# Performance work log

Measured on AMD Instinct MI355X. Metric: run time of the kernel, lower is better.

The kernel has to match this reference:

```python
import jax, jax.numpy as jnp
import numpy as np

HEAD_DIM = 64
R = 4            # region_token_num
THETA = 10000.0


def _rope_cos_sin(pos, D, theta):
    # pos: [B, L] int -> cos/sin [B, 1, L, D] (half-split / GPT-NeoX layout)
    inv_freq = theta ** (-(jnp.arange(0, D, 2, dtype=jnp.float32) / D))  # [D/2]
    ang = pos.astype(jnp.float32)[..., None] * inv_freq                  # [B, L, D/2]
    cos = jnp.concatenate([jnp.cos(ang), jnp.cos(ang)], axis=-1)[:, None]
    sin = jnp.concatenate([jnp.sin(ang), jnp.sin(ang)], axis=-1)[:, None]
    return cos, sin


def _apply_rope(x, cos, sin):
    # x: [B, H, L, D]
    D = x.shape[-1]
    x1, x2 = x[..., : D // 2], x[..., D // 2 :]
    rot = jnp.concatenate([-x2, x1], axis=-1)
    return x * cos + rot * sin


def _local_positions(regions):
    # index within contiguous region run: [B, T]
    B, T = regions.shape
    idx = jnp.arange(T, dtype=jnp.int32)
    is_new = jnp.concatenate(
        [jnp.ones((B, 1), bool), regions[:, 1:] != regions[:, :-1]], axis=1
    )
    start = jax.lax.cummax(jnp.where(is_new, idx[None, :], 0), axis=1)
    return idx[None, :] - start


def reference(query_q, x_k, x_v, regions, t_mask, n_mask, max_n):
    B, H, P, D = query_q.shape
    T = regions.shape[1]

    # ---- local RoPE positions: pool tokens all 0 (use_pool_offset=False),
    # x tokens: local index within region + R, zeroed on pads
    pool_pos = jnp.zeros((B, P), dtype=jnp.int32)
    x_pos = (_local_positions(regions) + R) * (regions > 0).astype(jnp.int32)

    cq, sq = _rope_cos_sin(pool_pos, D, THETA)
    ck, sk = _rope_cos_sin(x_pos, D, THETA)
    q = _apply_rope(query_q, cq, sq)
    k = _apply_rope(x_k, ck, sk)

    # ---- block-diagonal (same-region) cross-attention mask [B, 1, P, T]
    pool_region = jnp.repeat(jnp.arange(1, max_n + 1, dtype=regions.dtype), R)  # [P]
    pool_valid = jnp.repeat(n_mask, R, axis=1)                                   # [B, P]
    same = pool_region[None, :, None] == regions[:, None, :]
    valid = pool_valid[:, :, None] & t_mask[:, None, :]
    non_pad = (pool_region != 0)[None, :, None] & (regions != 0)[:, None, :]
    mask = (same & valid & non_pad)[:, None]                                     # [B,1,P,T]

    # ---- SDPA
    scale = 1.0 / jnp.sqrt(jnp.asarray(D, jnp.float32))
    scores = jnp.einsum('bhpd,bhtd->bhpt', q, k) * scale
    scores = jnp.where(mask, scores, jnp.asarray(-1e30, scores.dtype))
    attn = jax.nn.softmax(scores, axis=-1)
    return jnp.einsum('bhpt,bhtd->bhpd', attn, x_v)


def setup_inputs() -> dict:
    key = jax.random.key(0)
    k1, k2, k3, k4 = jax.random.split(key, 4)
    B, H, T, max_n = 4, 16, 4096, 64
    P = max_n * R
    regions = jnp.sort(jax.random.randint(k4, (B, T), 0, 65), axis=1)
    return {
        'query_q': jax.random.normal(k1, (B, H, P, HEAD_DIM), jnp.float32),
        'x_k': jax.random.normal(k2, (B, H, T, HEAD_DIM), jnp.float32),
        'x_v': jax.random.normal(k3, (B, H, T, HEAD_DIM), jnp.float32),
        'regions': regions,
        't_mask': jnp.ones((B, T), dtype=bool),
        'n_mask': jnp.ones((B, max_n), dtype=bool),
        'max_n': max_n,
    }
```

## Files before the change

kernel.cpp:

```cpp
#include <hip/hip_runtime.h>
#include <math.h>

#define NB   4
#define NH   16
#define NT   4096
#define ND   64
#define NP   256
#define NREG 64
#define RPOS 4

#define INVF_LOG2 0.4152410118609203f
#define QSCALE 0.18033688011112042f

__global__ void seg_kernel(const int* __restrict__ regions, int* __restrict__ bound) {
    const int b = blockIdx.x;
    const int* rb = regions + b * NT;
    int* bb = bound + b * 66;
    if (threadIdx.x < 66) bb[threadIdx.x] = NT;
    __syncthreads();
    for (int i = threadIdx.x; i < NT; i += blockDim.x) {
        const int r  = rb[i];
        const int rp = (i == 0) ? -1 : rb[i - 1];
        for (int v = rp + 1; v <= r; ++v) bb[v] = i;
    }
}

__global__ __launch_bounds__(256) void lca_kernel(
    const float* __restrict__ q,
    const float* __restrict__ k,
    const float* __restrict__ v,
    const int*   __restrict__ bound,
    float*       __restrict__ out)
{
    __shared__ float pacc[4][4][64];
    __shared__ float pl[4][4];

    const int tid  = threadIdx.x;
    const int wave = tid >> 6;
    const int lane = tid & 63;
    const int grp  = lane >> 3;
    const int li   = lane & 7;
    const int dlo  = li << 2;

    const int blk = blockIdx.x;
    const int rgp = blk & 31;
    const int h   = (blk >> 5) & (NH - 1);
    const int b   = blk >> 9;
    const int ri  = (rgp << 1) + (wave >> 1);
    const int w   = wave & 1;
    const int p0  = ri << 2;

    const size_t bh = (size_t)(b * NH + h);
    const float* kb = k + bh * (size_t)(NT * ND);
    const float* vb = v + bh * (size_t)(NT * ND);
    const float* qb = q + (bh * NP + p0) * ND;

    float qs[4][8];
    #pragma unroll
    for (int p = 0; p < 4; ++p) {
        const float4 qa = *(const float4*)(qb + p * ND + dlo);
        const float4 qc = *(const float4*)(qb + p * ND + 32 + dlo);
        qs[p][0] = qa.x * QSCALE; qs[p][1] = qa.y * QSCALE;
        qs[p][2] = qa.z * QSCALE; qs[p][3] = qa.w * QSCALE;
        qs[p][4] = qc.x * QSCALE; qs[p][5] = qc.y * QSCALE;
        qs[p][6] = qc.z * QSCALE; qs[p][7] = qc.w * QSCALE;
    }

    const int s   = bound[b * 66 + ri + 1];
    const int e   = bound[b * 66 + ri + 2];
    const int cnt = e - s;

    float l4[4] = {0.f, 0.f, 0.f, 0.f};
    float acc[4][8];
    #pragma unroll
    for (int p = 0; p < 4; ++p)
        #pragma unroll
        for (int i = 0; i < 8; ++i) acc[p][i] = 0.f;

    if (cnt > 0) {
        const int hlen  = ((cnt + 15) >> 4) << 3;
        const int ms    = s + w * hlen;
        const int me    = min(e, ms + hlen);
        const int mycnt = me - ms;
        if (mycnt > 0) {
            float frq[4];
            #pragma unroll
            for (int i = 0; i < 4; ++i)
                frq[i] = exp2f(-INVF_LOG2 * (float)(dlo + i));

            const int iters = (mycnt + 7) >> 3;

            const int t0c = min(ms + grp, e - 1);
            const float* kp = kb + (size_t)t0c * ND;
            const float* vp = vb + (size_t)t0c * ND;
            float4 ka = *(const float4*)(kp + dlo);
            float4 kc = *(const float4*)(kp + 32 + dlo);
            float4 va = *(const float4*)(vp + dlo);
            float4 vc = *(const float4*)(vp + 32 + dlo);

            for (int it = 0; it < iters; ++it) {
                const int tn = min(ms + ((it + 1) << 3) + grp, e - 1);
                const float* nkp = kb + (size_t)tn * ND;
                const float* nvp = vb + (size_t)tn * ND;
                const float4 nka = *(const float4*)(nkp + dlo);
                const float4 nkc = *(const float4*)(nkp + 32 + dlo);
                const float4 nva = *(const float4*)(nvp + dlo);
                const float4 nvc = *(const float4*)(nvp + 32 + dlo);

                const int   t     = ms + (it << 3) + grp;
                const bool  valid = t < me;
                const float pos   = (float)(min(t, e - 1) - s + RPOS);

                const float klo[4] = {ka.x, ka.y, ka.z, ka.w};
                const float khi[4] = {kc.x, kc.y, kc.z, kc.w};
                float pd0 = 0.f, pd1 = 0.f, pd2 = 0.f, pd3 = 0.f;
                #pragma unroll
                for (int i = 0; i < 4; ++i) {
                    float sa, ca;
                    __sincosf(pos * frq[i], &sa, &ca);
                    const float rlo = klo[i] * ca - khi[i] * sa;
                    const float rhi = khi[i] * ca + klo[i] * sa;
                    pd0 = fmaf(rlo, qs[0][i], fmaf(rhi, qs[0][i + 4], pd0));
                    pd1 = fmaf(rlo, qs[1][i], fmaf(rhi, qs[1][i + 4], pd1));
                    pd2 = fmaf(rlo, qs[2][i], fmaf(rhi, qs[2][i + 4], pd2));
                    pd3 = fmaf(rlo, qs[3][i], fmaf(rhi, qs[3][i + 4], pd3));
                }
                #pragma unroll
                for (int m = 1; m <= 4; m <<= 1) {
                    pd0 += __shfl_xor(pd0, m);
                    pd1 += __shfl_xor(pd1, m);
                    pd2 += __shfl_xor(pd2, m);
                    pd3 += __shfl_xor(pd3, m);
                }
                const float w0 = valid ? exp2f(pd0) : 0.f;
                const float w1 = valid ? exp2f(pd1) : 0.f;
                const float w2 = valid ? exp2f(pd2) : 0.f;
                const float w3 = valid ? exp2f(pd3) : 0.f;
                l4[0] += w0; l4[1] += w1; l4[2] += w2; l4[3] += w3;
                const float vx[8] = {va.x, va.y, va.z, va.w, vc.x, vc.y, vc.z, vc.w};
                #pragma unroll
                for (int i = 0; i < 8; ++i) {
                    acc[0][i] = fmaf(w0, vx[i], acc[0][i]);
                    acc[1][i] = fmaf(w1, vx[i], acc[1][i]);
                    acc[2][i] = fmaf(w2, vx[i], acc[2][i]);
                    acc[3][i] = fmaf(w3, vx[i], acc[3][i]);
                }
                ka = nka; kc = nkc; va = nva; vc = nvc;
            }
        }
    } else {
        for (int t = (w << 3) + grp; t < NT; t += 16) {
            const float* vp = vb + (size_t)t * ND;
            const float4 va = *(const float4*)(vp + dlo);
            const float4 vc = *(const float4*)(vp + 32 + dlo);
            acc[0][0] += va.x; acc[0][1] += va.y; acc[0][2] += va.z; acc[0][3] += va.w;
            acc[0][4] += vc.x; acc[0][5] += vc.y; acc[0][6] += vc.z; acc[0][7] += vc.w;
        }
        #pragma unroll
        for (int p = 1; p < 4; ++p)
            #pragma unroll
            for (int i = 0; i < 8; ++i) acc[p][i] = acc[0][i];
        l4[0] = l4[1] = l4[2] = l4[3] = (float)NT / 16.f;
    }

    #pragma unroll
    for (int m = 8; m <= 32; m <<= 1) {
        #pragma unroll
        for (int p = 0; p < 4; ++p) {
            l4[p] += __shfl_xor(l4[p], m);
            #pragma unroll
            for (int i = 0; i < 8; ++i) acc[p][i] += __shfl_xor(acc[p][i], m);
        }
    }

    if (grp == 0) {
        #pragma unroll
        for (int p = 0; p < 4; ++p) {
            *(float4*)&pacc[wave][p][dlo] =
                make_float4(acc[p][0], acc[p][1], acc[p][2], acc[p][3]);
            *(float4*)&pacc[wave][p][32 + dlo] =
                make_float4(acc[p][4], acc[p][5], acc[p][6], acc[p][7]);
        }
        if (li == 0) {
            #pragma unroll
            for (int p = 0; p < 4; ++p) pl[wave][p] = l4[p];
        }
    }
    __syncthreads();

    if (tid < 128) {
        const int rg2  = tid >> 6;
        const int pool = (tid >> 4) & 3;
        const int d    = (tid & 15) << 2;
        const int wA   = rg2 << 1, wB = wA + 1;
        const float lsum = pl[wA][pool] + pl[wB][pool];
        const float inv  = 1.f / lsum;
        const float4 a = *(const float4*)&pacc[wA][pool][d];
        const float4 c = *(const float4*)&pacc[wB][pool][d];
        const int   po = ((rgp << 1) + rg2) * 4 + pool;
        *(float4*)(out + (bh * NP + po) * ND + d) =
            make_float4((a.x + c.x) * inv, (a.y + c.y) * inv,
                        (a.z + c.z) * inv, (a.w + c.w) * inv);
    }
}

extern "C" void kernel_launch(void* const* d_in, const int* in_sizes, int n_in,
                              void* d_out, int out_size, void* d_ws, size_t ws_size,
                              hipStream_t stream) {
    (void)in_sizes; (void)n_in; (void)ws_size; (void)out_size;
    const float* q       = (const float*)d_in[0];
    const float* k       = (const float*)d_in[1];
    const float* v       = (const float*)d_in[2];
    const int*   regions = (const int*)d_in[3];
    float* out   = (float*)d_out;
    int*   bound = (int*)d_ws;

    seg_kernel<<<dim3(NB), 1024, 0, stream>>>(regions, bound);
    lca_kernel<<<dim3(NB * NH * (NREG / 2)), 256, 0, stream>>>(q, k, v, bound, out);
}
```

Measured before the change: 36.29 us.

## Assign one block per region with eight waves interleaving over tokens

Each block now handles a single region with 8 waves (512 threads) that stride across the region's tokens in an interleaved pattern, instead of two waves per region splitting the range in halves. The software prefetch of the next K/V rows is removed in favour of more waves in flight to hide latency, and the region bounds are broadcast through shared memory. This raises parallelism per region and balances the per-region work across waves, at the cost of a larger final reduction over 8 partial accumulators and more blocks and barriers.

```diff
diff --git a/kernel.cpp b/kernel.cpp
--- a/kernel.cpp
+++ b/kernel.cpp
@@ -8,6 +8,7 @@
 #define NP   256
 #define NREG 64
 #define RPOS 4
+#define NW   8
 
 #define INVF_LOG2 0.4152410118609203f
 #define QSCALE 0.18033688011112042f
@@ -25,35 +26,36 @@
     }
 }
 
-__global__ __launch_bounds__(256) void lca_kernel(
+__global__ __launch_bounds__(512) void lca_kernel(
     const float* __restrict__ q,
     const float* __restrict__ k,
     const float* __restrict__ v,
     const int*   __restrict__ bound,
     float*       __restrict__ out)
 {
-    __shared__ float pacc[4][4][64];
-    __shared__ float pl[4][4];
+    __shared__ int   sh_se[2];
+    __shared__ float pacc[NW][4][64];
+    __shared__ float pld[NW][4];
 
     const int tid  = threadIdx.x;
-    const int wave = tid >> 6;
+    const int w    = tid >> 6;
     const int lane = tid & 63;
     const int grp  = lane >> 3;
     const int li   = lane & 7;
     const int dlo  = li << 2;
 
     const int blk = blockIdx.x;
-    const int rgp = blk & 31;
-    const int h   = (blk >> 5) & (NH - 1);
-    const int b   = blk >> 9;
-    const int ri  = (rgp << 1) + (wave >> 1);
-    const int w   = wave & 1;
+    const int ri  = blk & (NREG - 1);
+    const int h   = (blk >> 6) & (NH - 1);
+    const int b   = blk >> 10;
     const int p0  = ri << 2;
 
     const size_t bh = (size_t)(b * NH + h);
     const float* kb = k + bh * (size_t)(NT * ND);
     const float* vb = v + bh * (size_t)(NT * ND);
     const float* qb = q + (bh * NP + p0) * ND;
+
+    if (tid < 2) sh_se[tid] = bound[b * 66 + ri + 1 + tid];
 
     float qs[4][8];
     #pragma unroll
@@ -66,8 +68,9 @@
         qs[p][6] = qc.z * QSCALE; qs[p][7] = qc.w * QSCALE;
     }
 
-    const int s   = bound[b * 66 + ri + 1];
-    const int e   = bound[b * 66 + ri + 2];
+    __syncthreads();
+    const int s   = sh_se[0];
+    const int e   = sh_se[1];
     const int cnt = e - s;
 
     float l4[4] = {0.f, 0.f, 0.f, 0.f};
@@ -78,78 +81,60 @@
         for (int i = 0; i < 8; ++i) acc[p][i] = 0.f;
 
     if (cnt > 0) {
-        const int hlen  = ((cnt + 15) >> 4) << 3;
-        const int ms    = s + w * hlen;
-        const int me    = min(e, ms + hlen);
-        const int mycnt = me - ms;
-        if (mycnt > 0) {
-            float frq[4];
-            #pragma unroll
-            for (int i = 0; i < 4; ++i)
-                frq[i] = exp2f(-INVF_LOG2 * (float)(dlo + i));
-
-            const int iters = (mycnt + 7) >> 3;
-
-            const int t0c = min(ms + grp, e - 1);
-            const float* kp = kb + (size_t)t0c * ND;
-            const float* vp = vb + (size_t)t0c * ND;
-            float4 ka = *(const float4*)(kp + dlo);
-            float4 kc = *(const float4*)(kp + 32 + dlo);
-            float4 va = *(const float4*)(vp + dlo);
-            float4 vc = *(const float4*)(vp + 32 + dlo);
-
-            for (int it = 0; it < iters; ++it) {
-                const int tn = min(ms + ((it + 1) << 3) + grp, e - 1);
-                const float* nkp = kb + (size_t)tn * ND;
-                const float* nvp = vb + (size_t)tn * ND;
-                const float4 nka = *(const float4*)(nkp + dlo);
-                const float4 nkc = *(const float4*)(nkp + 32 + dlo);
-                const float4 nva = *(const float4*)(nvp + dlo);
-                const float4 nvc = *(const float4*)(nvp + 32 + dlo);
-
-                const int   t     = ms + (it << 3) + grp;
-                const bool  valid = t < me;
-                const float pos   = (float)(min(t, e - 1) - s + RPOS);
-
-                const float klo[4] = {ka.x, ka.y, ka.z, ka.w};
-                const float khi[4] = {kc.x, kc.y, kc.z, kc.w};
-                float pd0 = 0.f, pd1 = 0.f, pd2 = 0.f, pd3 = 0.f;
-                #pragma unroll
-                for (int i = 0; i < 4; ++i) {
-                    float sa, ca;
-                    __sincosf(pos * frq[i], &sa, &ca);
-                    const float rlo = klo[i] * ca - khi[i] * sa;
-                    const float rhi = khi[i] * ca + klo[i] * sa;
-                    pd0 = fmaf(rlo, qs[0][i], fmaf(rhi, qs[0][i + 4], pd0));
-                    pd1 = fmaf(rlo, qs[1][i], fmaf(rhi, qs[1][i + 4], pd1));
-                    pd2 = fmaf(rlo, qs[2][i], fmaf(rhi, qs[2][i + 4], pd2));
-                    pd3 = fmaf(rlo, qs[3][i], fmaf(rhi, qs[3][i + 4], pd3));
-                }
-                #pragma unroll
-                for (int m = 1; m <= 4; m <<= 1) {
-                    pd0 += __shfl_xor(pd0, m);
-                    pd1 += __shfl_xor(pd1, m);
-                    pd2 += __shfl_xor(pd2, m);
-                    pd3 += __shfl_xor(pd3, m);
-                }
-                const float w0 = valid ? exp2f(pd0) : 0.f;
-                const float w1 = valid ? exp2f(pd1) : 0.f;
-                const float w2 = valid ? exp2f(pd2) : 0.f;
-                const float w3 = valid ? exp2f(pd3) : 0.f;
-                l4[0] += w0; l4[1] += w1; l4[2] += w2; l4[3] += w3;
-                const float vx[8] = {va.x, va.y, va.z, va.w, vc.x, vc.y, vc.z, vc.w};
-                #pragma unroll
-                for (int i = 0; i < 8; ++i) {
-                    acc[0][i] = fmaf(w0, vx[i], acc[0][i]);
-                    acc[1][i] = fmaf(w1, vx[i], acc[1][i]);
-                    acc[2][i] = fmaf(w2, vx[i], acc[2][i]);
-                    acc[3][i] = fmaf(w3, vx[i], acc[3][i]);
-                }
-                ka = nka; kc = nkc; va = nva; vc = nvc;
+        float frq[4];
+        #pragma unroll
+        for (int i = 0; i < 4; ++i)
+            frq[i] = exp2f(-INVF_LOG2 * (float)(dlo + i));
+
+        for (int ofs = w << 3; ofs < cnt; ofs += NW * 8) {
+            const int  off   = ofs + grp;
+            const bool valid = off < cnt;
+            const int  tc    = s + (valid ? off : cnt - 1);
+            const float* kp = kb + (size_t)tc * ND;
+            const float* vp = vb + (size_t)tc * ND;
+            const float4 ka = *(const float4*)(kp + dlo);
+            const float4 kc = *(const float4*)(kp + 32 + dlo);
+            const float4 va = *(const float4*)(vp + dlo);
+            const float4 vc = *(const float4*)(vp + 32 + dlo);
+
+            const float pos = (float)(off + RPOS);
+            const float klo[4] = {ka.x, ka.y, ka.z, ka.w};
+            const float khi[4] = {kc.x, kc.y, kc.z, kc.w};
+            float pd0 = 0.f, pd1 = 0.f, pd2 = 0.f, pd3 = 0.f;
+            #pragma unroll
+            for (int i = 0; i < 4; ++i) {
+                float sa, ca;
+                __sincosf(pos * frq[i], &sa, &ca);
+                const float rlo = klo[i] * ca - khi[i] * sa;
+                const float rhi = khi[i] * ca + klo[i] * sa;
+                pd0 = fmaf(rlo, qs[0][i], fmaf(rhi, qs[0][i + 4], pd0));
+                pd1 = fmaf(rlo, qs[1][i], fmaf(rhi, qs[1][i + 4], pd1));
+                pd2 = fmaf(rlo, qs[2][i], fmaf(rhi, qs[2][i + 4], pd2));
+                pd3 = fmaf(rlo, qs[3][i], fmaf(rhi, qs[3][i + 4], pd3));
             }
+            #pragma unroll
+            for (int m = 1; m <= 4; m <<= 1) {
+                pd0 += __shfl_xor(pd0, m);
+                pd1 += __shfl_xor(pd1, m);
+                pd2 += __shfl_xor(pd2, m);
+                pd3 += __shfl_xor(pd3, m);
+            }
+            const float w0 = valid ? exp2f(pd0) : 0.f;
+            const float w1 = valid ? exp2f(pd1) : 0.f;
+            const float w2 = valid ? exp2f(pd2) : 0.f;
+            const float w3 = valid ? exp2f(pd3) : 0.f;
+            l4[0] += w0; l4[1] += w1; l4[2] += w2; l4[3] += w3;
+            const float vx[8] = {va.x, va.y, va.z, va.w, vc.x, vc.y, vc.z, vc.w};
+            #pragma unroll
+            for (int i = 0; i < 8; ++i) {
+                acc[0][i] = fmaf(w0, vx[i], acc[0][i]);
+                acc[1][i] = fmaf(w1, vx[i], acc[1][i]);
+                acc[2][i] = fmaf(w2, vx[i], acc[2][i]);
+                acc[3][i] = fmaf(w3, vx[i], acc[3][i]);
+            }
         }
     } else {
-        for (int t = (w << 3) + grp; t < NT; t += 16) {
+        for (int t = (w << 3) + grp; t < NT; t += NW * 8) {
             const float* vp = vb + (size_t)t * ND;
             const float4 va = *(const float4*)(vp + dlo);
             const float4 vc = *(const float4*)(vp + 32 + dlo);
@@ -160,7 +145,7 @@
         for (int p = 1; p < 4; ++p)
             #pragma unroll
             for (int i = 0; i < 8; ++i) acc[p][i] = acc[0][i];
-        l4[0] = l4[1] = l4[2] = l4[3] = (float)NT / 16.f;
+        l4[0] = l4[1] = l4[2] = l4[3] = (float)NT / 64.f;
     }
 
     #pragma unroll
@@ -176,31 +161,32 @@
     if (grp == 0) {
         #pragma unroll
         for (int p = 0; p < 4; ++p) {
-            *(float4*)&pacc[wave][p][dlo] =
+            *(float4*)&pacc[w][p][dlo] =
                 make_float4(acc[p][0], acc[p][1], acc[p][2], acc[p][3]);
-            *(float4*)&pacc[wave][p][32 + dlo] =
+            *(float4*)&pacc[w][p][32 + dlo] =
                 make_float4(acc[p][4], acc[p][5], acc[p][6], acc[p][7]);
         }
         if (li == 0) {
             #pragma unroll
-            for (int p = 0; p < 4; ++p) pl[wave][p] = l4[p];
+            for (int p = 0; p < 4; ++p) pld[w][p] = l4[p];
         }
     }
     __syncthreads();
 
-    if (tid < 128) {
-        const int rg2  = tid >> 6;
-        const int pool = (tid >> 4) & 3;
+    if (tid < 64) {
+        const int pool = tid >> 4;
         const int d    = (tid & 15) << 2;
-        const int wA   = rg2 << 1, wB = wA + 1;
-        const float lsum = pl[wA][pool] + pl[wB][pool];
-        const float inv  = 1.f / lsum;
-        const float4 a = *(const float4*)&pacc[wA][pool][d];
-        const float4 c = *(const float4*)&pacc[wB][pool][d];
-        const int   po = ((rgp << 1) + rg2) * 4 + pool;
-        *(float4*)(out + (bh * NP + po) * ND + d) =
-            make_float4((a.x + c.x) * inv, (a.y + c.y) * inv,
-                        (a.z + c.z) * inv, (a.w + c.w) * inv);
+        float ls = 0.f;
+        float sx = 0.f, sy = 0.f, sz = 0.f, sw = 0.f;
+        #pragma unroll
+        for (int wv = 0; wv < NW; ++wv) {
+            ls += pld[wv][pool];
+            const float4 a = *(const float4*)&pacc[wv][pool][d];
+            sx += a.x; sy += a.y; sz += a.z; sw += a.w;
+        }
+        const float inv = 1.f / ls;
+        *(float4*)(out + (bh * NP + p0 + pool) * ND + d) =
+            make_float4(sx * inv, sy * inv, sz * inv, sw * inv);
     }
 }
 
@@ -216,5 +202,5 @@
     int*   bound = (int*)d_ws;
 
     seg_kernel<<<dim3(NB), 1024, 0, stream>>>(regions, bound);
-    lca_kernel<<<dim3(NB * NH * (NREG / 2)), 256, 0, stream>>>(q, k, v, bound, out);
+    lca_kernel<<<dim3(NB * NH * NREG), 512, 0, stream>>>(q, k, v, bound, out);
 }
```

Result: slower. 60.97 us (+68.0%).
